# Optimization experiments

Measured on AMD Instinct MI355X. Metric: run time of the kernel, lower is better.

Reference implementation:

```python
import jax, jax.numpy as jnp
import numpy as np

N_EMBD = 1024
HEAD_SIZE = 64


def setup_inputs() -> dict:
    key = jax.random.key(0)
    k1, k2, k3, k4 = jax.random.split(key, 4)
    x = jax.random.normal(k1, (8, 2048, N_EMBD), dtype=jnp.float32)
    # torch Linear(n_embd, head_size, bias=False): y = x @ W.T with W [out,in].
    # Store as [in, out] so y = x @ W. Scale init like torch default (~1/sqrt(in)).
    s = 1.0 / np.sqrt(N_EMBD)
    Wk = jax.random.uniform(k2, (N_EMBD, HEAD_SIZE), jnp.float32, -s, s)
    Wq = jax.random.uniform(k3, (N_EMBD, HEAD_SIZE), jnp.float32, -s, s)
    Wv = jax.random.uniform(k4, (N_EMBD, HEAD_SIZE), jnp.float32, -s, s)
    return {"x": x, "Wk": Wk, "Wq": Wq, "Wv": Wv}


def reference(x, Wk, Wq, Wv):
    # x: [B,T,C]
    B, T, C = x.shape
    k = x @ Wk  # [B,T,H]
    q = x @ Wq  # [B,T,H]
    v = x @ Wv  # [B,T,H]
    scale = HEAD_SIZE ** -0.5
    wei = jnp.einsum('bth,bsh->bts', q, k) * scale  # [B,T,T]
    causal = jnp.tril(jnp.ones((T, T), dtype=bool))  # [T,T]
    wei = jnp.where(causal[None, :, :], wei, -jnp.inf)
    wei = jax.nn.softmax(wei, axis=-1)
    # dropout(p=0.2) is identity in eval mode (deterministic baseline)
    out = jnp.einsum('bts,bsh->bth', wei, v)  # [B,T,H]
    return out
```

## Files before the change

kernel.cpp:

```cpp
#include <hip/hip_runtime.h>
#include <hip/hip_bf16.h>

#define B_DIM 8
#define T_DIM 2048
#define C_DIM 1024
#define H_DIM 64
#define BT (B_DIM * T_DIM)

typedef __attribute__((ext_vector_type(8))) short bf16x8;
typedef __attribute__((ext_vector_type(4))) float f32x4;

__device__ __forceinline__ ushort f2bf(float f) {
    __hip_bfloat16 h = __float2bfloat16(f);
    return *reinterpret_cast<ushort*>(&h);
}
__device__ __forceinline__ unsigned int packbf(float a, float b) {
    return (unsigned int)f2bf(a) | ((unsigned int)f2bf(b) << 16);
}

__global__ __launch_bounds__(256) void wt_convert_kernel(
    const float* __restrict__ Wk, const float* __restrict__ Wq,
    const float* __restrict__ Wv, ushort* __restrict__ wt)
{
    const int n = blockIdx.x;
    const float* src = (n < 64) ? Wk : (n < 128) ? Wq : Wv;
    const float scale = (n >= 64 && n < 128) ? 0.125f * 1.4426950408889634f : 1.0f;
    const int col = n & 63;
    for (int k = threadIdx.x; k < C_DIM; k += 256)
        wt[(size_t)n * C_DIM + k] = f2bf(src[(size_t)k * H_DIM + col] * scale);
}

__global__ __launch_bounds__(256) void qkv_gemm_kernel(
    const float* __restrict__ x, const ushort* __restrict__ wt,
    ushort* __restrict__ kb, ushort* __restrict__ qb, ushort* __restrict__ vt)
{
    __shared__ ushort Xf[2][4 * 64 * 8];
    const int tid = threadIdx.x;
    const int wave = tid >> 6, lane = tid & 63;
    const int col = lane & 15, quad = lane >> 4;
    const int r0 = blockIdx.x * 32;

    f32x4 acc[2][3];
    #pragma unroll
    for (int m = 0; m < 2; ++m)
        #pragma unroll
        for (int i = 0; i < 3; ++i) acc[m][i] = (f32x4){0.f, 0.f, 0.f, 0.f};

    const int xrow = (wave >> 1) * 16 + col;
    const int xcc  = (wave & 1) * 4 + quad;
    const float* xsrc = x + (size_t)(r0 + xrow) * C_DIM + xcc * 8;

    const ushort* wsrc[3][2];
    #pragma unroll
    for (int j = 0; j < 3; ++j)
        #pragma unroll
        for (int ks = 0; ks < 2; ++ks)
            wsrc[j][ks] = wt + (size_t)((wave * 3 + j) * 16 + col) * C_DIM
                             + ks * 32 + quad * 8;

    {
        const float4 f0 = *(const float4*)(xsrc);
        const float4 f1 = *(const float4*)(xsrc + 4);
        uint4 u;
        u.x = packbf(f0.x, f0.y); u.y = packbf(f0.z, f0.w);
        u.z = packbf(f1.x, f1.y); u.w = packbf(f1.z, f1.w);
        *(uint4*)&Xf[0][(wave * 64 + lane) * 8] = u;
    }
    bf16x8 wcur[3][2];
    #pragma unroll
    for (int j = 0; j < 3; ++j)
        #pragma unroll
        for (int ks = 0; ks < 2; ++ks)
            wcur[j][ks] = *(const bf16x8*)(wsrc[j][ks]);
    __syncthreads();

    for (int i = 0; i < 16; ++i) {
        const int b = i & 1;
        bf16x8 wnxt[3][2];
        float4 nf0, nf1;
        if (i < 15) {
            const int k1 = (i + 1) * 64;
            #pragma unroll
            for (int j = 0; j < 3; ++j)
                #pragma unroll
                for (int ks = 0; ks < 2; ++ks)
                    wnxt[j][ks] = *(const bf16x8*)(wsrc[j][ks] + k1);
            nf0 = *(const float4*)(xsrc + k1);
            nf1 = *(const float4*)(xsrc + k1 + 4);
        }
        #pragma unroll
        for (int ks = 0; ks < 2; ++ks) {
            const bf16x8 a0 = *(const bf16x8*)&Xf[b][((    ks) * 64 + lane) * 8];
            const bf16x8 a1 = *(const bf16x8*)&Xf[b][((2 + ks) * 64 + lane) * 8];
            #pragma unroll
            for (int j = 0; j < 3; ++j) {
                acc[0][j] = __builtin_amdgcn_mfma_f32_16x16x32_bf16(a0, wcur[j][ks], acc[0][j], 0, 0, 0);
                acc[1][j] = __builtin_amdgcn_mfma_f32_16x16x32_bf16(a1, wcur[j][ks], acc[1][j], 0, 0, 0);
            }
        }
        if (i < 15) {
            #pragma unroll
            for (int j = 0; j < 3; ++j)
                #pragma unroll
                for (int ks = 0; ks < 2; ++ks)
                    wcur[j][ks] = wnxt[j][ks];
            uint4 u;
            u.x = packbf(nf0.x, nf0.y); u.y = packbf(nf0.z, nf0.w);
            u.z = packbf(nf1.x, nf1.y); u.w = packbf(nf1.z, nf1.w);
            *(uint4*)&Xf[b ^ 1][(wave * 64 + lane) * 8] = u;
        }
        __syncthreads();
    }

    #pragma unroll
    for (int i = 0; i < 3; ++i) {
        const int nt = wave * 3 + i;
        #pragma unroll
        for (int mf = 0; mf < 2; ++mf) {
            const int rbase = r0 + mf * 16 + quad * 4;
            if (nt < 4) {
                const int n = nt * 16 + col;
                #pragma unroll
                for (int r = 0; r < 4; ++r)
                    kb[(size_t)(rbase + r) * H_DIM + n] = f2bf(acc[mf][i][r]);
            } else if (nt < 8) {
                const int n = nt * 16 + col - 64;
                #pragma unroll
                for (int r = 0; r < 4; ++r)
                    qb[(size_t)(rbase + r) * H_DIM + n] = f2bf(acc[mf][i][r]);
            } else {
                const int h = nt * 16 + col - 128;
                const int vbatch = rbase >> 11, vrow = rbase & (T_DIM - 1);
                ushort u4[4] = {f2bf(acc[mf][i][0]), f2bf(acc[mf][i][1]),
                                f2bf(acc[mf][i][2]), f2bf(acc[mf][i][3])};
                unsigned long long uu; __builtin_memcpy(&uu, u4, 8);
                *(unsigned long long*)(vt + ((size_t)vbatch * H_DIM + h) * T_DIM + vrow) = uu;
            }
        }
    }
}

__global__ __launch_bounds__(256) void attn_kernel(
    const ushort* __restrict__ kb, const ushort* __restrict__ qb,
    const ushort* __restrict__ vt, float* __restrict__ out)
{
    __shared__ unsigned int Ps[4][16 * 34];
    __shared__ float Om[4][64][17];
    __shared__ float Mm[4][16], Lm[4][16];

    const int tid = threadIdx.x;
    const int wave = tid >> 6, lane = tid & 63;
    const int col = lane & 15, quad = lane >> 4;
    const int batch = blockIdx.x & 7;
    const int qtile = 127 - (blockIdx.x >> 3);
    const int q0 = qtile * 16;

    const ushort* kbase = kb + (size_t)batch * T_DIM * H_DIM;
    const ushort* vbase = vt + (size_t)batch * H_DIM * T_DIM;

    const size_t qoff = (size_t)(batch * T_DIM + q0 + col) * H_DIM + quad * 8;
    const bf16x8 bq0 = *(const bf16x8*)(qb + qoff);
    const bf16x8 bq1 = *(const bf16x8*)(qb + qoff + 32);

    float m_ = -INFINITY, l_ = 0.f;
    f32x4 o_[4];
    #pragma unroll
    for (int i = 0; i < 4; ++i) o_[i] = (f32x4){0.f, 0.f, 0.f, 0.f};

    const int ntiles = (q0 + 16 + 63) >> 6;
    unsigned int* psw = &Ps[wave][0];

    for (int t = wave; t < ntiles; t += 4) {
        const int kb0 = t * 64;
        f32x4 s[4];
        #pragma unroll
        for (int mt = 0; mt < 4; ++mt) s[mt] = (f32x4){0.f, 0.f, 0.f, 0.f};
        #pragma unroll
        for (int ks = 0; ks < 2; ++ks) {
            const bf16x8 bq = ks ? bq1 : bq0;
            #pragma unroll
            for (int mt = 0; mt < 4; ++mt) {
                const bf16x8 ak = *(const bf16x8*)
                    (kbase + (size_t)(kb0 + mt * 16 + col) * H_DIM + ks * 32 + quad * 8);
                s[mt] = __builtin_amdgcn_mfma_f32_16x16x32_bf16(ak, bq, s[mt], 0, 0, 0);
            }
        }
        if (kb0 + 63 > q0) {
            const int kq = kb0 + quad * 4 - q0 - col;
            #pragma unroll
            for (int mt = 0; mt < 4; ++mt)
                #pragma unroll
                for (int reg = 0; reg < 4; ++reg)
                    if (kq + mt * 16 + reg > 0) s[mt][reg] = -INFINITY;
        }
        float mr = -INFINITY;
        #pragma unroll
        for (int mt = 0; mt < 4; ++mt)
            #pragma unroll
            for (int reg = 0; reg < 4; ++reg) mr = fmaxf(mr, s[mt][reg]);
        mr = fmaxf(mr, __shfl_xor(mr, 16));
        mr = fmaxf(mr, __shfl_xor(mr, 32));
        const float mn = fmaxf(m_, mr);
        const float corr = exp2f(m_ - mn);
        float sum = 0.f;
        #pragma unroll
        for (int mt = 0; mt < 4; ++mt)
            #pragma unroll
            for (int reg = 0; reg < 4; ++reg) {
                const float pv = exp2f(s[mt][reg] - mn);
                s[mt][reg] = pv;
                sum += pv;
            }
        sum += __shfl_xor(sum, 16);
        sum += __shfl_xor(sum, 32);
        l_ = l_ * corr + sum;
        m_ = mn;
        #pragma unroll
        for (int ht = 0; ht < 4; ++ht) o_[ht] *= corr;
        #pragma unroll
        for (int mt = 0; mt < 4; ++mt) {
            uint2 w2;
            w2.x = packbf(s[mt][0], s[mt][1]);
            w2.y = packbf(s[mt][2], s[mt][3]);
            *(uint2*)&psw[col * 34 + mt * 8 + quad * 2] = w2;
        }
        #pragma unroll
        for (int ks2 = 0; ks2 < 2; ++ks2) {
            const uint2 ra = *(const uint2*)&psw[col * 34 + ks2 * 16 + quad * 4];
            const uint2 rb = *(const uint2*)&psw[col * 34 + ks2 * 16 + quad * 4 + 2];
            unsigned int ub[4] = {ra.x, ra.y, rb.x, rb.y};
            bf16x8 bp; __builtin_memcpy(&bp, ub, 16);
            #pragma unroll
            for (int ht = 0; ht < 4; ++ht) {
                const bf16x8 av = *(const bf16x8*)
                    (vbase + (size_t)(ht * 16 + col) * T_DIM + kb0 + ks2 * 32 + quad * 8);
                o_[ht] = __builtin_amdgcn_mfma_f32_16x16x32_bf16(av, bp, o_[ht], 0, 0, 0);
            }
        }
    }

    #pragma unroll
    for (int ht = 0; ht < 4; ++ht)
        #pragma unroll
        for (int reg = 0; reg < 4; ++reg)
            Om[wave][ht * 16 + quad * 4 + reg][col] = o_[ht][reg];
    if (lane < 16) { Mm[wave][lane] = m_; Lm[wave][lane] = l_; }
    __syncthreads();
    {
        const int q = tid >> 4, hb = tid & 15;
        const float M = fmaxf(fmaxf(Mm[0][q], Mm[1][q]), fmaxf(Mm[2][q], Mm[3][q]));
        const float a0 = exp2f(Mm[0][q] - M), a1 = exp2f(Mm[1][q] - M);
        const float a2 = exp2f(Mm[2][q] - M), a3 = exp2f(Mm[3][q] - M);
        const float L = Lm[0][q] * a0 + Lm[1][q] * a1 + Lm[2][q] * a2 + Lm[3][q] * a3;
        const float rL = 1.0f / L;
        float* orow = out + (size_t)(batch * T_DIM + q0 + q) * H_DIM;
        #pragma unroll
        for (int i = 0; i < 4; ++i) {
            const int h = hb + 16 * i;
            orow[h] = (Om[0][h][q] * a0 + Om[1][h][q] * a1 +
                       Om[2][h][q] * a2 + Om[3][h][q] * a3) * rL;
        }
    }
}

extern "C" void kernel_launch(void* const* d_in, const int* in_sizes, int n_in,
                              void* d_out, int out_size, void* d_ws, size_t ws_size,
                              hipStream_t stream)
{
    const float* x  = (const float*)d_in[0];
    const float* Wk = (const float*)d_in[1];
    const float* Wq = (const float*)d_in[2];
    const float* Wv = (const float*)d_in[3];

    ushort* kbuf = (ushort*)d_ws;
    ushort* qbuf = kbuf + (size_t)BT * H_DIM;
    ushort* vtb  = qbuf + (size_t)BT * H_DIM;
    ushort* wt   = vtb  + (size_t)BT * H_DIM;

    wt_convert_kernel<<<192, 256, 0, stream>>>(Wk, Wq, Wv, wt);
    qkv_gemm_kernel<<<BT / 32, 256, 0, stream>>>(x, wt, kbuf, qbuf, vtb);
    attn_kernel<<<B_DIM * 128, 256, 0, stream>>>(kbuf, qbuf, vtb, (float*)d_out);
}
```

Baseline: 156.4 us.

## Split QKV GEMM K across wave groups and dual-tile attention loop

The QKV projection kernel now runs 512 threads, with two wave groups each covering half of the K dimension. Their partial accumulators are reduced through shared memory before the bf16 stores, which halves the serial K loop per block. The attention kernel processes two key tiles per wave iteration with independent softmax states (A/B), merged at the end, to expose more MFMA and memory-level parallelism. The costs are extra LDS use, an added sync and reduction step, and higher register pressure under the new launch bounds.

```diff
diff --git a/kernel.cpp b/kernel.cpp
--- a/kernel.cpp
+++ b/kernel.cpp
@@ -30,33 +30,37 @@
         wt[(size_t)n * C_DIM + k] = f2bf(src[(size_t)k * H_DIM + col] * scale);
 }
 
-__global__ __launch_bounds__(256) void qkv_gemm_kernel(
+__global__ __launch_bounds__(512, 4) void qkv_gemm_kernel(
     const float* __restrict__ x, const ushort* __restrict__ wt,
     ushort* __restrict__ kb, ushort* __restrict__ qb, ushort* __restrict__ vt)
 {
-    __shared__ ushort Xf[2][4 * 64 * 8];
+    __shared__ ushort Xf[2][2][4 * 64 * 8];
+    __shared__ float  Ls[256 * 25];
     const int tid = threadIdx.x;
     const int wave = tid >> 6, lane = tid & 63;
+    const int kh = wave >> 2, nh = wave & 3;
     const int col = lane & 15, quad = lane >> 4;
     const int r0 = blockIdx.x * 32;
+    const int kbase = kh * 512;
 
     f32x4 acc[2][3];
     #pragma unroll
     for (int m = 0; m < 2; ++m)
         #pragma unroll
-        for (int i = 0; i < 3; ++i) acc[m][i] = (f32x4){0.f, 0.f, 0.f, 0.f};
-
-    const int xrow = (wave >> 1) * 16 + col;
-    const int xcc  = (wave & 1) * 4 + quad;
-    const float* xsrc = x + (size_t)(r0 + xrow) * C_DIM + xcc * 8;
+        for (int j = 0; j < 3; ++j) acc[m][j] = (f32x4){0.f, 0.f, 0.f, 0.f};
+
+    const float* xsrc = x + (size_t)(r0 + (nh >> 1) * 16 + col) * C_DIM
+                          + kbase + (nh & 1) * 32 + quad * 8;
+    ushort* xdst[2] = {&Xf[0][kh][(nh * 64 + lane) * 8],
+                       &Xf[1][kh][(nh * 64 + lane) * 8]};
 
     const ushort* wsrc[3][2];
     #pragma unroll
     for (int j = 0; j < 3; ++j)
         #pragma unroll
         for (int ks = 0; ks < 2; ++ks)
-            wsrc[j][ks] = wt + (size_t)((wave * 3 + j) * 16 + col) * C_DIM
-                             + ks * 32 + quad * 8;
+            wsrc[j][ks] = wt + (size_t)((nh * 3 + j) * 16 + col) * C_DIM
+                             + kbase + ks * 32 + quad * 8;
 
     {
         const float4 f0 = *(const float4*)(xsrc);
@@ -64,7 +68,7 @@
         uint4 u;
         u.x = packbf(f0.x, f0.y); u.y = packbf(f0.z, f0.w);
         u.z = packbf(f1.x, f1.y); u.w = packbf(f1.z, f1.w);
-        *(uint4*)&Xf[0][(wave * 64 + lane) * 8] = u;
+        *(uint4*)xdst[0] = u;
     }
     bf16x8 wcur[3][2];
     #pragma unroll
@@ -74,11 +78,11 @@
             wcur[j][ks] = *(const bf16x8*)(wsrc[j][ks]);
     __syncthreads();
 
-    for (int i = 0; i < 16; ++i) {
+    for (int i = 0; i < 8; ++i) {
         const int b = i & 1;
         bf16x8 wnxt[3][2];
         float4 nf0, nf1;
-        if (i < 15) {
+        if (i < 7) {
             const int k1 = (i + 1) * 64;
             #pragma unroll
             for (int j = 0; j < 3; ++j)
@@ -88,17 +92,20 @@
             nf0 = *(const float4*)(xsrc + k1);
             nf1 = *(const float4*)(xsrc + k1 + 4);
         }
-        #pragma unroll
-        for (int ks = 0; ks < 2; ++ks) {
-            const bf16x8 a0 = *(const bf16x8*)&Xf[b][((    ks) * 64 + lane) * 8];
-            const bf16x8 a1 = *(const bf16x8*)&Xf[b][((2 + ks) * 64 + lane) * 8];
+        bf16x8 a[2][2];
+        #pragma unroll
+        for (int mf = 0; mf < 2; ++mf)
+            #pragma unroll
+            for (int ks = 0; ks < 2; ++ks)
+                a[mf][ks] = *(const bf16x8*)&Xf[b][kh][((mf * 2 + ks) * 64 + lane) * 8];
+        #pragma unroll
+        for (int ks = 0; ks < 2; ++ks)
             #pragma unroll
             for (int j = 0; j < 3; ++j) {
-                acc[0][j] = __builtin_amdgcn_mfma_f32_16x16x32_bf16(a0, wcur[j][ks], acc[0][j], 0, 0, 0);
-                acc[1][j] = __builtin_amdgcn_mfma_f32_16x16x32_bf16(a1, wcur[j][ks], acc[1][j], 0, 0, 0);
-            }
-        }
-        if (i < 15) {
+                acc[0][j] = __builtin_amdgcn_mfma_f32_16x16x32_bf16(a[0][ks], wcur[j][ks], acc[0][j], 0, 0, 0);
+                acc[1][j] = __builtin_amdgcn_mfma_f32_16x16x32_bf16(a[1][ks], wcur[j][ks], acc[1][j], 0, 0, 0);
+            }
+        if (i < 7) {
             #pragma unroll
             for (int j = 0; j < 3; ++j)
                 #pragma unroll
@@ -107,44 +114,66 @@
             uint4 u;
             u.x = packbf(nf0.x, nf0.y); u.y = packbf(nf0.z, nf0.w);
             u.z = packbf(nf1.x, nf1.y); u.w = packbf(nf1.z, nf1.w);
-            *(uint4*)&Xf[b ^ 1][(wave * 64 + lane) * 8] = u;
+            *(uint4*)xdst[b ^ 1] = u;
         }
         __syncthreads();
     }
 
-    #pragma unroll
-    for (int i = 0; i < 3; ++i) {
-        const int nt = wave * 3 + i;
-        #pragma unroll
-        for (int mf = 0; mf < 2; ++mf) {
-            const int rbase = r0 + mf * 16 + quad * 4;
-            if (nt < 4) {
-                const int n = nt * 16 + col;
+    if (kh == 1) {
+        float* dst = &Ls[(tid & 255) * 25];
+        #pragma unroll
+        for (int mf = 0; mf < 2; ++mf)
+            #pragma unroll
+            for (int j = 0; j < 3; ++j)
                 #pragma unroll
                 for (int r = 0; r < 4; ++r)
-                    kb[(size_t)(rbase + r) * H_DIM + n] = f2bf(acc[mf][i][r]);
-            } else if (nt < 8) {
-                const int n = nt * 16 + col - 64;
+                    dst[(mf * 3 + j) * 4 + r] = acc[mf][j][r];
+    }
+    __syncthreads();
+    if (kh == 0) {
+        const float* srcl = &Ls[tid * 25];
+        #pragma unroll
+        for (int mf = 0; mf < 2; ++mf)
+            #pragma unroll
+            for (int j = 0; j < 3; ++j)
                 #pragma unroll
                 for (int r = 0; r < 4; ++r)
-                    qb[(size_t)(rbase + r) * H_DIM + n] = f2bf(acc[mf][i][r]);
-            } else {
-                const int h = nt * 16 + col - 128;
-                const int vbatch = rbase >> 11, vrow = rbase & (T_DIM - 1);
-                ushort u4[4] = {f2bf(acc[mf][i][0]), f2bf(acc[mf][i][1]),
-                                f2bf(acc[mf][i][2]), f2bf(acc[mf][i][3])};
-                unsigned long long uu; __builtin_memcpy(&uu, u4, 8);
-                *(unsigned long long*)(vt + ((size_t)vbatch * H_DIM + h) * T_DIM + vrow) = uu;
-            }
-        }
-    }
-}
-
-__global__ __launch_bounds__(256) void attn_kernel(
+                    acc[mf][j][r] += srcl[(mf * 3 + j) * 4 + r];
+
+        #pragma unroll
+        for (int j = 0; j < 3; ++j) {
+            const int nt = nh * 3 + j;
+            #pragma unroll
+            for (int mf = 0; mf < 2; ++mf) {
+                const int rbase = r0 + mf * 16 + quad * 4;
+                if (nt < 4) {
+                    const int n = nt * 16 + col;
+                    #pragma unroll
+                    for (int r = 0; r < 4; ++r)
+                        kb[(size_t)(rbase + r) * H_DIM + n] = f2bf(acc[mf][j][r]);
+                } else if (nt < 8) {
+                    const int n = nt * 16 + col - 64;
+                    #pragma unroll
+                    for (int r = 0; r < 4; ++r)
+                        qb[(size_t)(rbase + r) * H_DIM + n] = f2bf(acc[mf][j][r]);
+                } else {
+                    const int h = nt * 16 + col - 128;
+                    const int vbatch = rbase >> 11, vrow = rbase & (T_DIM - 1);
+                    ushort u4[4] = {f2bf(acc[mf][j][0]), f2bf(acc[mf][j][1]),
+                                    f2bf(acc[mf][j][2]), f2bf(acc[mf][j][3])};
+                    unsigned long long uu; __builtin_memcpy(&uu, u4, 8);
+                    *(unsigned long long*)(vt + ((size_t)vbatch * H_DIM + h) * T_DIM + vrow) = uu;
+                }
+            }
+        }
+    }
+}
+
+__global__ __launch_bounds__(256, 4) void attn_kernel(
     const ushort* __restrict__ kb, const ushort* __restrict__ qb,
     const ushort* __restrict__ vt, float* __restrict__ out)
 {
-    __shared__ unsigned int Ps[4][16 * 34];
+    __shared__ unsigned int Ps[8][16 * 34];
     __shared__ float Om[4][64][17];
     __shared__ float Mm[4][16], Lm[4][16];
 
@@ -162,17 +191,17 @@
     const bf16x8 bq0 = *(const bf16x8*)(qb + qoff);
     const bf16x8 bq1 = *(const bf16x8*)(qb + qoff + 32);
 
-    float m_ = -INFINITY, l_ = 0.f;
-    f32x4 o_[4];
-    #pragma unroll
-    for (int i = 0; i < 4; ++i) o_[i] = (f32x4){0.f, 0.f, 0.f, 0.f};
+    float mA = -INFINITY, lA = 0.f, mB = -INFINITY, lB = 0.f;
+    f32x4 oA[4], oB[4];
+    #pragma unroll
+    for (int i = 0; i < 4; ++i) {
+        oA[i] = (f32x4){0.f, 0.f, 0.f, 0.f};
+        oB[i] = (f32x4){0.f, 0.f, 0.f, 0.f};
+    }
 
     const int ntiles = (q0 + 16 + 63) >> 6;
-    unsigned int* psw = &Ps[wave][0];
-
-    for (int t = wave; t < ntiles; t += 4) {
-        const int kb0 = t * 64;
-        f32x4 s[4];
+
+    auto qk_tile = [&](int kb0, f32x4* s) {
         #pragma unroll
         for (int mt = 0; mt < 4; ++mt) s[mt] = (f32x4){0.f, 0.f, 0.f, 0.f};
         #pragma unroll
@@ -193,6 +222,10 @@
                 for (int reg = 0; reg < 4; ++reg)
                     if (kq + mt * 16 + reg > 0) s[mt][reg] = -INFINITY;
         }
+    };
+
+    auto sm_pv = [&](int kb0, f32x4* s, float& m_, float& l_, f32x4* o_,
+                     unsigned int* psw) {
         float mr = -INFINITY;
         #pragma unroll
         for (int mt = 0; mt < 4; ++mt)
@@ -237,22 +270,36 @@
                 o_[ht] = __builtin_amdgcn_mfma_f32_16x16x32_bf16(av, bp, o_[ht], 0, 0, 0);
             }
         }
-    }
-
+    };
+
+    for (int t = wave; t < ntiles; t += 8) {
+        const int t2 = t + 4;
+        const bool hasB = t2 < ntiles;
+        f32x4 sA[4], sB[4];
+        qk_tile(t * 64, sA);
+        if (hasB) qk_tile(t2 * 64, sB);
+        sm_pv(t * 64, sA, mA, lA, oA, &Ps[wave][0]);
+        if (hasB) sm_pv(t2 * 64, sB, mB, lB, oB, &Ps[wave + 4][0]);
+    }
+
+    const float M = fmaxf(mA, mB);
+    const float eA = (mA == -INFINITY) ? 0.f : exp2f(mA - M);
+    const float eB = (mB == -INFINITY) ? 0.f : exp2f(mB - M);
+    const float L = lA * eA + lB * eB;
     #pragma unroll
     for (int ht = 0; ht < 4; ++ht)
         #pragma unroll
         for (int reg = 0; reg < 4; ++reg)
-            Om[wave][ht * 16 + quad * 4 + reg][col] = o_[ht][reg];
-    if (lane < 16) { Mm[wave][lane] = m_; Lm[wave][lane] = l_; }
+            Om[wave][ht * 16 + quad * 4 + reg][col] = oA[ht][reg] * eA + oB[ht][reg] * eB;
+    if (lane < 16) { Mm[wave][lane] = M; Lm[wave][lane] = L; }
     __syncthreads();
     {
         const int q = tid >> 4, hb = tid & 15;
-        const float M = fmaxf(fmaxf(Mm[0][q], Mm[1][q]), fmaxf(Mm[2][q], Mm[3][q]));
-        const float a0 = exp2f(Mm[0][q] - M), a1 = exp2f(Mm[1][q] - M);
-        const float a2 = exp2f(Mm[2][q] - M), a3 = exp2f(Mm[3][q] - M);
-        const float L = Lm[0][q] * a0 + Lm[1][q] * a1 + Lm[2][q] * a2 + Lm[3][q] * a3;
-        const float rL = 1.0f / L;
+        const float Mb = fmaxf(fmaxf(Mm[0][q], Mm[1][q]), fmaxf(Mm[2][q], Mm[3][q]));
+        const float a0 = exp2f(Mm[0][q] - Mb), a1 = exp2f(Mm[1][q] - Mb);
+        const float a2 = exp2f(Mm[2][q] - Mb), a3 = exp2f(Mm[3][q] - Mb);
+        const float Lb = Lm[0][q] * a0 + Lm[1][q] * a1 + Lm[2][q] * a2 + Lm[3][q] * a3;
+        const float rL = 1.0f / Lb;
         float* orow = out + (size_t)(batch * T_DIM + q0 + q) * H_DIM;
         #pragma unroll
         for (int i = 0; i < 4; ++i) {
@@ -278,6 +325,6 @@
     ushort* wt   = vtb  + (size_t)BT * H_DIM;
 
     wt_convert_kernel<<<192, 256, 0, stream>>>(Wk, Wq, Wv, wt);
-    qkv_gemm_kernel<<<BT / 32, 256, 0, stream>>>(x, wt, kbuf, qbuf, vtb);
+    qkv_gemm_kernel<<<BT / 32, 512, 0, stream>>>(x, wt, kbuf, qbuf, vtb);
     attn_kernel<<<B_DIM * 128, 256, 0, stream>>>(kbuf, qbuf, vtb, (float*)d_out);
 }
```

New measurement: 162.9 us. 1.04x slower.
